# Kernel optimization log

Hardware: AMD Instinct MI355X
Metric: run time of the kernel (lower is better)

The kernel has to match this reference:

```python
import jax, jax.numpy as jnp
import numpy as np

D_MODEL = 1024
N_HEADS = 16
D_K = D_MODEL // N_HEADS
B, N_Q, N_KV = 2, 2048, 2048


def setup_inputs() -> dict:
    key = jax.random.key(0)
    ks = jax.random.split(key, 13)
    s = 1.0 / np.sqrt(D_MODEL)
    Q = jax.random.normal(ks[0], (B, N_Q, D_MODEL), dtype=jnp.float32)
    K = jax.random.normal(ks[1], (B, N_KV, D_MODEL), dtype=jnp.float32)
    V = jax.random.normal(ks[2], (B, N_KV, D_MODEL), dtype=jnp.float32)
    mask = jax.random.uniform(ks[3], (B, N_KV)) > 0.1
    mask = mask.at[:, 0].set(True)  # ensure at least one valid kv per batch
    Wq = jax.random.uniform(ks[4], (D_MODEL, D_MODEL), minval=-s, maxval=s)
    bq = jax.random.uniform(ks[5], (D_MODEL,), minval=-s, maxval=s)
    Wk = jax.random.uniform(ks[6], (D_MODEL, D_MODEL), minval=-s, maxval=s)
    bk = jax.random.uniform(ks[7], (D_MODEL,), minval=-s, maxval=s)
    Wv = jax.random.uniform(ks[8], (D_MODEL, D_MODEL), minval=-s, maxval=s)
    bv = jax.random.uniform(ks[9], (D_MODEL,), minval=-s, maxval=s)
    Wo = jax.random.uniform(ks[10], (D_MODEL, D_MODEL), minval=-s, maxval=s)
    bo = jax.random.uniform(ks[11], (D_MODEL,), minval=-s, maxval=s)
    return {"Q": Q, "K": K, "V": V, "mask": mask,
            "Wq": Wq, "bq": bq, "Wk": Wk, "bk": bk,
            "Wv": Wv, "bv": bv, "Wo": Wo, "bo": bo}


def reference(Q, K, V, mask, Wq, bq, Wk, bk, Wv, bv, Wo, bo):
    Bsz, nq, _ = Q.shape
    nkv = K.shape[1]
    # torch Linear: y = x @ W.T + b
    q = (Q @ Wq.T + bq).reshape(Bsz, nq, N_HEADS, D_K).transpose(0, 2, 1, 3)
    k = (K @ Wk.T + bk).reshape(Bsz, nkv, N_HEADS, D_K).transpose(0, 2, 1, 3)
    v = (V @ Wv.T + bv).reshape(Bsz, nkv, N_HEADS, D_K).transpose(0, 2, 1, 3)
    scores = jnp.einsum('bhqd,bhkd->bhqk', q, k) / jnp.sqrt(jnp.float32(D_K))
    scores = jnp.where(mask[:, None, None, :], scores, -jnp.inf)
    attn = jax.nn.softmax(scores, axis=-1)  # dropout p=0 (eval) -> identity
    out = jnp.einsum('bhqk,bhkd->bhqd', attn, v)
    out = out.transpose(0, 2, 1, 3).reshape(Bsz, nq, D_MODEL)
    return (out @ Wo.T + bo, attn)
```

## Files before the change

### kernel.cpp

```cpp
#include <hip/hip_runtime.h>
#include <math.h>

#define H 16
#define DK 64
#define NSEQ 2048
#define DM 1024
#define BSZ 2

typedef float f32x4 __attribute__((ext_vector_type(4)));
typedef short bf16x8 __attribute__((ext_vector_type(8)));
typedef unsigned short u16;

__device__ __forceinline__ u16 f2bf(float f) {
    unsigned int u = __float_as_uint(f);
    u += 0x7fffu + ((u >> 16) & 1u);
    return (u16)(u >> 16);
}
__device__ __forceinline__ float bf2f(u16 h) {
    return __uint_as_float(((unsigned int)h) << 16);
}

__global__ __launch_bounds__(256)
void cvt4_bf16(const float* __restrict__ s0, const float* __restrict__ s1,
               const float* __restrict__ s2, const float* __restrict__ s3,
               u16* __restrict__ dst) {
    const int sel = blockIdx.x >> 10;
    const float* s = sel == 0 ? s0 : sel == 1 ? s1 : sel == 2 ? s2 : s3;
    const int i = ((blockIdx.x & 1023) * 256 + threadIdx.x) * 4;
    float4 v = *(const float4*)(&s[i]);
    ushort4 o = make_ushort4(f2bf(v.x), f2bf(v.y), f2bf(v.z), f2bf(v.w));
    *(ushort4*)(&dst[(size_t)sel * DM * DM + i]) = o;
}

__global__ __launch_bounds__(1024, 4)
void gemm_qkv(const float* __restrict__ Qs_, const float* __restrict__ Ks_,
              const float* __restrict__ Vs_,
              const u16* __restrict__ Wqb, const u16* __restrict__ Wkb,
              const u16* __restrict__ Wvb,
              const float* __restrict__ bq, const float* __restrict__ bk,
              const float* __restrict__ bv,
              u16* __restrict__ qd, u16* __restrict__ kd, u16* __restrict__ vt) {
    __shared__ __align__(16) u16 At[64 * 1024];

    const int which = blockIdx.x >> 6;
    const int mblk  = blockIdx.x & 63;
    const float* A    = which == 0 ? Qs_ : which == 1 ? Ks_ : Vs_;
    const u16*   Wb   = which == 0 ? Wqb : which == 1 ? Wkb : Wvb;
    const float* bias = which == 0 ? bq  : which == 1 ? bk  : bv;

    const int tid  = threadIdx.x;
    const int lane = tid & 63;
    const int w    = tid >> 6;
    const int m0   = mblk * 64;

    {
        const int row = tid & 63;
        const int kg  = tid >> 6;
#pragma unroll
        for (int i = 0; i < 8; ++i) {
            int k = kg * 64 + i * 8;
            float4 a0 = *(const float4*)(&A[(size_t)(m0 + row) * 1024 + k]);
            float4 a1 = *(const float4*)(&A[(size_t)(m0 + row) * 1024 + k + 4]);
            bf16x8 pv;
            pv[0] = (short)f2bf(a0.x); pv[1] = (short)f2bf(a0.y);
            pv[2] = (short)f2bf(a0.z); pv[3] = (short)f2bf(a0.w);
            pv[4] = (short)f2bf(a1.x); pv[5] = (short)f2bf(a1.y);
            pv[6] = (short)f2bf(a1.z); pv[7] = (short)f2bf(a1.w);
            int slot = (kg * 8 + i) ^ (row & 7);
            *(bf16x8*)(&At[row * 1024 + slot * 8]) = pv;
        }
    }
    __syncthreads();

    const int fr = lane & 15;
    const int fg = lane >> 4;

    f32x4 acc[4][4];
#pragma unroll
    for (int rf = 0; rf < 4; ++rf)
#pragma unroll
        for (int ct = 0; ct < 4; ++ct) acc[rf][ct] = {0.f, 0.f, 0.f, 0.f};

    const int nbase = w * 64;
    for (int ks = 0; ks < 32; ++ks) {
        int slot = (ks * 4 + fg) ^ (fr & 7);
        bf16x8 aA[4];
#pragma unroll
        for (int rf = 0; rf < 4; ++rf)
            aA[rf] = *(const bf16x8*)(&At[(rf * 16 + fr) * 1024 + slot * 8]);
#pragma unroll
        for (int ct = 0; ct < 4; ++ct) {
            bf16x8 bB = *(const bf16x8*)(&Wb[(size_t)(nbase + ct * 16 + fr) * 1024 + ks * 32 + fg * 8]);
#pragma unroll
            for (int rf = 0; rf < 4; ++rf)
                acc[rf][ct] = __builtin_amdgcn_mfma_f32_16x16x32_bf16(aA[rf], bB, acc[rf][ct], 0, 0, 0);
        }
    }

    const int b = m0 >> 11;
    if (which == 2) {
#pragma unroll
        for (int ct = 0; ct < 4; ++ct) {
            int n = nbase + ct * 16 + fr;
            float bvv = bias[n];
            int hh = n >> 6, d = n & 63;
            size_t base = ((size_t)(b * H + hh)) * DK * NSEQ + (size_t)d * NSEQ;
#pragma unroll
            for (int rf = 0; rf < 4; ++rf) {
                int kv = (m0 & 2047) + rf * 16 + fg * 4;
                ushort4 pk = make_ushort4(f2bf(acc[rf][ct][0] + bvv), f2bf(acc[rf][ct][1] + bvv),
                                          f2bf(acc[rf][ct][2] + bvv), f2bf(acc[rf][ct][3] + bvv));
                *(ushort4*)(&vt[base + kv]) = pk;
            }
        }
    } else {
        u16* C = which == 0 ? qd : kd;
#pragma unroll
        for (int ct = 0; ct < 4; ++ct) {
            int n = nbase + ct * 16 + fr;
            float bvv = bias[n];
            int hh = n >> 6, d = n & 63;
#pragma unroll
            for (int rf = 0; rf < 4; ++rf)
#pragma unroll
                for (int reg = 0; reg < 4; ++reg) {
                    int nq = (m0 & 2047) + rf * 16 + fg * 4 + reg;
                    C[(((size_t)(b * H + hh)) * NSEQ + nq) * DK + d] = f2bf(acc[rf][ct][reg] + bvv);
                }
        }
    }
}

__global__ __launch_bounds__(256)
void gemm_out(const u16* __restrict__ Ab, const u16* __restrict__ Wb,
              const float* __restrict__ bias, float* __restrict__ Cdst) {
    __shared__ __align__(16) char smem[16 * 1028 * 4];
    u16* At = (u16*)smem;

    const int tid  = threadIdx.x;
    const int lane = tid & 63;
    const int w    = tid >> 6;
    const int m0   = blockIdx.x * 16;

    {
        const int row = tid & 15;
        const int kg  = tid >> 4;
#pragma unroll
        for (int i = 0; i < 8; ++i) {
            int k = kg * 64 + i * 8;
            bf16x8 pv = *(const bf16x8*)(&Ab[(size_t)(m0 + row) * 1024 + k]);
            int slot = (kg * 8 + i) ^ (row & 7);
            *(bf16x8*)(&At[row * 1024 + slot * 8]) = pv;
        }
    }
    __syncthreads();

    const int fr = lane & 15;
    const int fg = lane >> 4;

    f32x4 acc[16];
#pragma unroll
    for (int ct = 0; ct < 16; ++ct) acc[ct] = {0.f, 0.f, 0.f, 0.f};

    const int nbase = w * 256;
    for (int ks = 0; ks < 32; ++ks) {
        int slot = (ks * 4 + fg) ^ (fr & 7);
        bf16x8 aA = *(const bf16x8*)(&At[fr * 1024 + slot * 8]);
#pragma unroll
        for (int ct = 0; ct < 16; ++ct) {
            bf16x8 bB = *(const bf16x8*)(&Wb[(size_t)(nbase + ct * 16 + fr) * 1024 + ks * 32 + fg * 8]);
            acc[ct] = __builtin_amdgcn_mfma_f32_16x16x32_bf16(aA, bB, acc[ct], 0, 0, 0);
        }
    }

    __syncthreads();
    float* Ct = (float*)smem;
    const int r4 = fg * 4;
#pragma unroll
    for (int ct = 0; ct < 16; ++ct) {
        int n = nbase + ct * 16 + fr;
        float bvv = bias[n];
#pragma unroll
        for (int reg = 0; reg < 4; ++reg)
            Ct[(r4 + reg) * 1028 + n] = acc[ct][reg] + bvv;
    }
    __syncthreads();
#pragma unroll
    for (int rr = 0; rr < 4; ++rr) {
        int row = w * 4 + rr;
#pragma unroll
        for (int seg = 0; seg < 4; ++seg) {
            int c = seg * 256 + lane * 4;
            f32x4 v = *(const f32x4*)(&Ct[row * 1028 + c]);
            *(f32x4*)(&Cdst[(size_t)(m0 + row) * 1024 + c]) = v;
        }
    }
}

__global__ __launch_bounds__(512, 2)
void attn_mfma(const u16* __restrict__ qb, const u16* __restrict__ kb,
               const u16* __restrict__ vt, const int* __restrict__ mask,
               float* __restrict__ attn, u16* __restrict__ ao) {
    __shared__ __align__(16) u16 Pband[32][2056];
    __shared__ unsigned Mbits[64];
    __shared__ float Sws[8][32];
    __shared__ float Sinv[32];

    const int tid  = threadIdx.x;
    const int lane = tid & 63;
    const int w    = tid >> 6;
    const int fr   = lane & 15;
    const int fg   = lane >> 4;

    const int bid = blockIdx.x;
    const int wg  = (bid & 7) * 256 + (bid >> 3);
    const int bh  = wg >> 6;
    const int qt  = wg & 63;
    const int b   = bh / H, h = bh % H;
    const int q0  = qt * 32;

    const u16* qh = qb + (size_t)bh * NSEQ * DK;
    const u16* kh = kb + (size_t)bh * NSEQ * DK;
    const u16* vh = vt + (size_t)bh * DK * NSEQ;

#pragma unroll
    for (int j = 0; j < 4; ++j) {
        int kv = j * 512 + w * 64 + lane;
        unsigned long long bal = __ballot(mask[b * NSEQ + kv] != 0);
        if (lane == 0) {
            Mbits[j * 16 + w * 2]     = (unsigned)bal;
            Mbits[j * 16 + w * 2 + 1] = (unsigned)(bal >> 32);
        }
    }

    bf16x8 aQ[2][2];
#pragma unroll
    for (int qs = 0; qs < 2; ++qs)
#pragma unroll
        for (int ks = 0; ks < 2; ++ks)
            aQ[qs][ks] = *(const bf16x8*)(&qh[(size_t)(q0 + qs * 16 + fr) * DK + ks * 32 + fg * 8]);

    const int col0 = w * 32 + fr;
    const int col1 = col0 + 16;

    __syncthreads();

    unsigned mb0 = 0, mb1 = 0;
#pragma unroll
    for (int st = 0; st < 8; ++st) {
        unsigned word = Mbits[st * 8 + w];
        mb0 |= ((word >> fr) & 1u) << st;
        mb1 |= ((word >> (16 + fr)) & 1u) << st;
    }

    float sum[2][4] = {};
    f32x4 accO[2][4];
#pragma unroll
    for (int qs = 0; qs < 2; ++qs)
#pragma unroll
        for (int g = 0; g < 4; ++g) accO[qs][g] = {0.f, 0.f, 0.f, 0.f};
    const float scale = 0.125f;

    bf16x8 bK0c[2], bK1c[2];
#pragma unroll
    for (int ks = 0; ks < 2; ++ks) {
        bK0c[ks] = *(const bf16x8*)(&kh[(size_t)col0 * DK + ks * 32 + fg * 8]);
        bK1c[ks] = *(const bf16x8*)(&kh[(size_t)col1 * DK + ks * 32 + fg * 8]);
    }

    for (int st = 0; st < 8; ++st) {
        const int cb = st * 256;

        bf16x8 bV[4];
#pragma unroll
        for (int g = 0; g < 4; ++g)
            bV[g] = *(const bf16x8*)(&vh[(size_t)(g * 16 + fr) * NSEQ + cb + w * 32 + fg * 8]);

        const int stn = (st < 7) ? st + 1 : 7;
        bf16x8 bK0n[2], bK1n[2];
#pragma unroll
        for (int ks = 0; ks < 2; ++ks) {
            bK0n[ks] = *(const bf16x8*)(&kh[(size_t)(stn * 256 + col0) * DK + ks * 32 + fg * 8]);
            bK1n[ks] = *(const bf16x8*)(&kh[(size_t)(stn * 256 + col1) * DK + ks * 32 + fg * 8]);
        }

        __builtin_amdgcn_s_setprio(1);
        f32x4 s0[2], s1[2];
#pragma unroll
        for (int qs = 0; qs < 2; ++qs) { s0[qs] = {0.f,0.f,0.f,0.f}; s1[qs] = {0.f,0.f,0.f,0.f}; }
#pragma unroll
        for (int qs = 0; qs < 2; ++qs)
#pragma unroll
            for (int ks = 0; ks < 2; ++ks) {
                s0[qs] = __builtin_amdgcn_mfma_f32_16x16x32_bf16(aQ[qs][ks], bK0c[ks], s0[qs], 0, 0, 0);
                s1[qs] = __builtin_amdgcn_mfma_f32_16x16x32_bf16(aQ[qs][ks], bK1c[ks], s1[qs], 0, 0, 0);
            }
        __builtin_amdgcn_s_setprio(0);

        const bool m0 = (mb0 >> st) & 1, m1 = (mb1 >> st) & 1;
#pragma unroll
        for (int qs = 0; qs < 2; ++qs)
#pragma unroll
            for (int reg = 0; reg < 4; ++reg) {
                float e0 = m0 ? __expf(s0[qs][reg] * scale) : 0.f;
                float e1 = m1 ? __expf(s1[qs][reg] * scale) : 0.f;
                sum[qs][reg] += e0 + e1;
                Pband[qs * 16 + fg * 4 + reg][cb + col0] = f2bf(e0);
                Pband[qs * 16 + fg * 4 + reg][cb + col1] = f2bf(e1);
            }

        asm volatile("s_waitcnt lgkmcnt(0)" ::: "memory");
        bf16x8 aP[2];
#pragma unroll
        for (int qs = 0; qs < 2; ++qs)
            aP[qs] = *(const bf16x8*)(&Pband[qs * 16 + fr][cb + w * 32 + fg * 8]);

        __builtin_amdgcn_s_setprio(1);
#pragma unroll
        for (int qs = 0; qs < 2; ++qs)
#pragma unroll
            for (int g = 0; g < 4; ++g)
                accO[qs][g] = __builtin_amdgcn_mfma_f32_16x16x32_bf16(aP[qs], bV[g], accO[qs][g], 0, 0, 0);
        __builtin_amdgcn_s_setprio(0);

#pragma unroll
        for (int ks = 0; ks < 2; ++ks) { bK0c[ks] = bK0n[ks]; bK1c[ks] = bK1n[ks]; }
    }

#pragma unroll
    for (int off = 1; off < 16; off <<= 1) {
#pragma unroll
        for (int qs = 0; qs < 2; ++qs)
#pragma unroll
            for (int reg = 0; reg < 4; ++reg)
                sum[qs][reg] += __shfl_xor(sum[qs][reg], off);
    }
    if (fr == 0) {
#pragma unroll
        for (int qs = 0; qs < 2; ++qs)
#pragma unroll
            for (int reg = 0; reg < 4; ++reg)
                Sws[w][qs * 16 + fg * 4 + reg] = sum[qs][reg];
    }
    __syncthreads();
    if (tid < 32) {
        float s = 0.f;
#pragma unroll
        for (int wv = 0; wv < 8; ++wv) s += Sws[wv][tid];
        Sinv[tid] = 1.0f / s;
    }
    __syncthreads();

#pragma unroll
    for (int rr = 0; rr < 4; ++rr) {
        int row = w * 4 + rr;
        float inv = Sinv[row];
        float* dst = attn + ((size_t)bh * NSEQ + q0 + row) * NSEQ;
#pragma unroll
        for (int seg = 0; seg < 8; ++seg) {
            int c = seg * 256 + lane * 4;
            ushort4 pv = *(const ushort4*)(&Pband[row][c]);
            f32x4 o = { bf2f(pv.x) * inv, bf2f(pv.y) * inv,
                        bf2f(pv.z) * inv, bf2f(pv.w) * inv };
            *(f32x4*)(&dst[c]) = o;
        }
    }
    __syncthreads();

    float* Of = (float*)Pband;
#pragma unroll
    for (int qs = 0; qs < 2; ++qs)
#pragma unroll
        for (int g = 0; g < 4; ++g)
#pragma unroll
            for (int reg = 0; reg < 4; ++reg)
                Of[(w * 32 + qs * 16 + fg * 4 + reg) * 68 + g * 16 + fr] = accO[qs][g][reg];
    __syncthreads();
    {
        int row = tid >> 4, cq = (tid & 15) * 4;
        f32x4 o = {0.f, 0.f, 0.f, 0.f};
#pragma unroll
        for (int wv = 0; wv < 8; ++wv)
            o += *(const f32x4*)(&Of[(wv * 32 + row) * 68 + cq]);
        float inv = Sinv[row];
        ushort4 st4 = make_ushort4(f2bf(o[0] * inv), f2bf(o[1] * inv),
                                   f2bf(o[2] * inv), f2bf(o[3] * inv));
        *(ushort4*)(&ao[((size_t)(b * NSEQ + q0 + row)) * DM + h * DK + cq]) = st4;
    }
}

extern "C" void kernel_launch(void* const* d_in, const int* in_sizes, int n_in,
                              void* d_out, int out_size, void* d_ws, size_t ws_size,
                              hipStream_t stream) {
    const float* Q    = (const float*)d_in[0];
    const float* K    = (const float*)d_in[1];
    const float* V    = (const float*)d_in[2];
    const int*   mask = (const int*)  d_in[3];
    const float* Wq   = (const float*)d_in[4];
    const float* bq   = (const float*)d_in[5];
    const float* Wk   = (const float*)d_in[6];
    const float* bk   = (const float*)d_in[7];
    const float* Wv   = (const float*)d_in[8];
    const float* bv   = (const float*)d_in[9];
    const float* Wo   = (const float*)d_in[10];
    const float* bo   = (const float*)d_in[11];

    float* out  = (float*)d_out;
    float* attn = out + (size_t)BSZ * NSEQ * DM;

    u16* Wqb = (u16*)d_ws;
    u16* Wkb = Wqb + (size_t)DM * DM;
    u16* Wvb = Wkb + (size_t)DM * DM;
    u16* Wob = Wvb + (size_t)DM * DM;
    u16* qbp = Wob + (size_t)DM * DM;
    u16* kbp = qbp + (size_t)BSZ * NSEQ * DM;
    u16* vbp = kbp + (size_t)BSZ * NSEQ * DM;
    u16* aob = vbp + (size_t)BSZ * NSEQ * DM;
    u16* vtb = aob + (size_t)BSZ * NSEQ * DM;

    cvt4_bf16<<<dim3(4096), dim3(256), 0, stream>>>(Wq, Wk, Wv, Wo, Wqb);

    gemm_qkv<<<dim3(192), dim3(1024), 0, stream>>>(Q, K, V, Wqb, Wkb, Wvb,
                                                   bq, bk, bv, qbp, kbp, vtb);

    attn_mfma<<<dim3(BSZ * H * (NSEQ / 32)), dim3(512), 0, stream>>>(qbp, kbp, vtb, mask, attn, aob);

    gemm_out<<<dim3(BSZ * NSEQ / 16), dim3(256), 0, stream>>>(aob, Wob, bo, out);
}
```

Measured before the change: 375.2 us.

## Split attention into a row-sum pass and a recompute pass with a small LDS stage

Measured after the change: 415.4 us. 1.11x slower.

```diff
diff --git a/kernel.cpp b/kernel.cpp
--- a/kernel.cpp
+++ b/kernel.cpp
@@ -197,14 +197,17 @@
     }
 }
 
-__global__ __launch_bounds__(512, 2)
+#define PST 260
+__global__ __launch_bounds__(512, 4)
 void attn_mfma(const u16* __restrict__ qb, const u16* __restrict__ kb,
                const u16* __restrict__ vt, const int* __restrict__ mask,
                float* __restrict__ attn, u16* __restrict__ ao) {
-    __shared__ __align__(16) u16 Pband[32][2056];
+    __shared__ __align__(16) char lds[256 * 66 * 4];
     __shared__ unsigned Mbits[64];
     __shared__ float Sws[8][32];
     __shared__ float Sinv[32];
+
+    float* stage = (float*)lds;
 
     const int tid  = threadIdx.x;
     const int lane = tid & 63;
@@ -235,38 +238,92 @@
 
     bf16x8 aQ[2][2];
 #pragma unroll
-    for (int qs = 0; qs < 2; ++qs)
+    for (int qg = 0; qg < 2; ++qg)
 #pragma unroll
         for (int ks = 0; ks < 2; ++ks)
-            aQ[qs][ks] = *(const bf16x8*)(&qh[(size_t)(q0 + qs * 16 + fr) * DK + ks * 32 + fg * 8]);
-
-    const int col0 = w * 32 + fr;
-    const int col1 = col0 + 16;
-
-    __syncthreads();
-
-    unsigned mb0 = 0, mb1 = 0;
-#pragma unroll
-    for (int st = 0; st < 8; ++st) {
-        unsigned word = Mbits[st * 8 + w];
-        mb0 |= ((word >> fr) & 1u) << st;
-        mb1 |= ((word >> (16 + fr)) & 1u) << st;
-    }
-
-    float sum[2][4] = {};
+            aQ[qg][ks] = *(const bf16x8*)(&qh[(size_t)(q0 + qg * 16 + fr) * DK + ks * 32 + fg * 8]);
+
+    __syncthreads();
+
+    const float scale = 0.125f;
+    const int slab = w * 32;
+
+    float sum[2] = {0.f, 0.f};
+    {
+        bf16x8 aKc[2][2], aKn[2][2];
+#pragma unroll
+        for (int kvb = 0; kvb < 2; ++kvb)
+#pragma unroll
+            for (int ks = 0; ks < 2; ++ks)
+                aKc[kvb][ks] = *(const bf16x8*)(&kh[(size_t)(slab + kvb * 16 + fr) * DK + ks * 32 + fg * 8]);
+
+        for (int st = 0; st < 8; ++st) {
+            const int stn = (st < 7) ? st + 1 : 7;
+#pragma unroll
+            for (int kvb = 0; kvb < 2; ++kvb)
+#pragma unroll
+                for (int ks = 0; ks < 2; ++ks)
+                    aKn[kvb][ks] = *(const bf16x8*)(&kh[(size_t)(stn * 256 + slab + kvb * 16 + fr) * DK + ks * 32 + fg * 8]);
+
+            __builtin_amdgcn_s_setprio(1);
+            f32x4 s[2][2];
+#pragma unroll
+            for (int qg = 0; qg < 2; ++qg)
+#pragma unroll
+                for (int kvb = 0; kvb < 2; ++kvb) {
+                    s[qg][kvb] = {0.f, 0.f, 0.f, 0.f};
+#pragma unroll
+                    for (int ks = 0; ks < 2; ++ks)
+                        s[qg][kvb] = __builtin_amdgcn_mfma_f32_16x16x32_bf16(aKc[kvb][ks], aQ[qg][ks], s[qg][kvb], 0, 0, 0);
+                }
+            __builtin_amdgcn_s_setprio(0);
+
+            const unsigned word = Mbits[st * 8 + w];
+#pragma unroll
+            for (int qg = 0; qg < 2; ++qg)
+#pragma unroll
+                for (int kvb = 0; kvb < 2; ++kvb)
+#pragma unroll
+                    for (int reg = 0; reg < 4; ++reg) {
+                        bool mm = (word >> (kvb * 16 + fg * 4 + reg)) & 1u;
+                        sum[qg] += mm ? __expf(s[qg][kvb][reg] * scale) : 0.f;
+                    }
+#pragma unroll
+            for (int kvb = 0; kvb < 2; ++kvb)
+#pragma unroll
+                for (int ks = 0; ks < 2; ++ks) aKc[kvb][ks] = aKn[kvb][ks];
+        }
+    }
+
+#pragma unroll
+    for (int off = 16; off < 64; off <<= 1) {
+#pragma unroll
+        for (int qg = 0; qg < 2; ++qg)
+            sum[qg] += __shfl_xor(sum[qg], off);
+    }
+    if (fg == 0) {
+#pragma unroll
+        for (int qg = 0; qg < 2; ++qg)
+            Sws[w][qg * 16 + fr] = sum[qg];
+    }
+    __syncthreads();
+    if (tid < 32) {
+        float s = 0.f;
+#pragma unroll
+        for (int wv = 0; wv < 8; ++wv) s += Sws[wv][tid];
+        Sinv[tid] = 1.0f / s;
+    }
+    __syncthreads();
+
+    float sinv[2];
+#pragma unroll
+    for (int qg = 0; qg < 2; ++qg) sinv[qg] = Sinv[qg * 16 + fr];
+
     f32x4 accO[2][4];
 #pragma unroll
-    for (int qs = 0; qs < 2; ++qs)
-#pragma unroll
-        for (int g = 0; g < 4; ++g) accO[qs][g] = {0.f, 0.f, 0.f, 0.f};
-    const float scale = 0.125f;
-
-    bf16x8 bK0c[2], bK1c[2];
-#pragma unroll
-    for (int ks = 0; ks < 2; ++ks) {
-        bK0c[ks] = *(const bf16x8*)(&kh[(size_t)col0 * DK + ks * 32 + fg * 8]);
-        bK1c[ks] = *(const bf16x8*)(&kh[(size_t)col1 * DK + ks * 32 + fg * 8]);
-    }
+    for (int qg = 0; qg < 2; ++qg)
+#pragma unroll
+        for (int g = 0; g < 4; ++g) accO[qg][g] = {0.f, 0.f, 0.f, 0.f};
 
     for (int st = 0; st < 8; ++st) {
         const int cb = st * 256;
@@ -274,117 +331,91 @@
         bf16x8 bV[4];
 #pragma unroll
         for (int g = 0; g < 4; ++g)
-            bV[g] = *(const bf16x8*)(&vh[(size_t)(g * 16 + fr) * NSEQ + cb + w * 32 + fg * 8]);
-
-        const int stn = (st < 7) ? st + 1 : 7;
-        bf16x8 bK0n[2], bK1n[2];
-#pragma unroll
-        for (int ks = 0; ks < 2; ++ks) {
-            bK0n[ks] = *(const bf16x8*)(&kh[(size_t)(stn * 256 + col0) * DK + ks * 32 + fg * 8]);
-            bK1n[ks] = *(const bf16x8*)(&kh[(size_t)(stn * 256 + col1) * DK + ks * 32 + fg * 8]);
-        }
+            bV[g] = *(const bf16x8*)(&vh[(size_t)(g * 16 + fr) * NSEQ + cb + slab + fg * 8]);
+
+        bf16x8 aK[2][2];
+#pragma unroll
+        for (int kvb = 0; kvb < 2; ++kvb)
+#pragma unroll
+            for (int ks = 0; ks < 2; ++ks)
+                aK[kvb][ks] = *(const bf16x8*)(&kh[(size_t)(cb + slab + kvb * 16 + fr) * DK + ks * 32 + fg * 8]);
 
         __builtin_amdgcn_s_setprio(1);
-        f32x4 s0[2], s1[2];
-#pragma unroll
-        for (int qs = 0; qs < 2; ++qs) { s0[qs] = {0.f,0.f,0.f,0.f}; s1[qs] = {0.f,0.f,0.f,0.f}; }
-#pragma unroll
-        for (int qs = 0; qs < 2; ++qs)
-#pragma unroll
-            for (int ks = 0; ks < 2; ++ks) {
-                s0[qs] = __builtin_amdgcn_mfma_f32_16x16x32_bf16(aQ[qs][ks], bK0c[ks], s0[qs], 0, 0, 0);
-                s1[qs] = __builtin_amdgcn_mfma_f32_16x16x32_bf16(aQ[qs][ks], bK1c[ks], s1[qs], 0, 0, 0);
+        f32x4 s[2][2];
+#pragma unroll
+        for (int qg = 0; qg < 2; ++qg)
+#pragma unroll
+            for (int kvb = 0; kvb < 2; ++kvb) {
+                s[qg][kvb] = {0.f, 0.f, 0.f, 0.f};
+#pragma unroll
+                for (int ks = 0; ks < 2; ++ks)
+                    s[qg][kvb] = __builtin_amdgcn_mfma_f32_16x16x32_bf16(aK[kvb][ks], aQ[qg][ks], s[qg][kvb], 0, 0, 0);
             }
         __builtin_amdgcn_s_setprio(0);
 
-        const bool m0 = (mb0 >> st) & 1, m1 = (mb1 >> st) & 1;
-#pragma unroll
-        for (int qs = 0; qs < 2; ++qs)
-#pragma unroll
-            for (int reg = 0; reg < 4; ++reg) {
-                float e0 = m0 ? __expf(s0[qs][reg] * scale) : 0.f;
-                float e1 = m1 ? __expf(s1[qs][reg] * scale) : 0.f;
-                sum[qs][reg] += e0 + e1;
-                Pband[qs * 16 + fg * 4 + reg][cb + col0] = f2bf(e0);
-                Pband[qs * 16 + fg * 4 + reg][cb + col1] = f2bf(e1);
+        const unsigned word = Mbits[st * 8 + w];
+#pragma unroll
+        for (int qg = 0; qg < 2; ++qg) {
+            const int row = qg * 16 + fr;
+            const int sw  = (row & 7) << 2;
+#pragma unroll
+            for (int kvb = 0; kvb < 2; ++kvb) {
+                f32x4 ev;
+#pragma unroll
+                for (int reg = 0; reg < 4; ++reg) {
+                    bool mm = (word >> (kvb * 16 + fg * 4 + reg)) & 1u;
+                    ev[reg] = mm ? __expf(s[qg][kvb][reg] * scale) * sinv[qg] : 0.f;
+                }
+                int col = (slab + kvb * 16 + fg * 4) ^ sw;
+                *(f32x4*)(&stage[row * PST + col]) = ev;
             }
-
-        asm volatile("s_waitcnt lgkmcnt(0)" ::: "memory");
-        bf16x8 aP[2];
-#pragma unroll
-        for (int qs = 0; qs < 2; ++qs)
-            aP[qs] = *(const bf16x8*)(&Pband[qs * 16 + fr][cb + w * 32 + fg * 8]);
+        }
+        __syncthreads();
+
+#pragma unroll
+        for (int rr = 0; rr < 4; ++rr) {
+            int row = w * 4 + rr;
+            int sw  = (row & 7) << 2;
+            f32x4 v = *(const f32x4*)(&stage[row * PST + ((lane * 4) ^ sw)]);
+            *(f32x4*)(&attn[((size_t)bh * NSEQ + q0 + row) * NSEQ + cb + lane * 4]) = v;
+        }
 
         __builtin_amdgcn_s_setprio(1);
 #pragma unroll
-        for (int qs = 0; qs < 2; ++qs)
+        for (int qg = 0; qg < 2; ++qg) {
+            const int row = qg * 16 + fr;
+            const int sw  = (row & 7) << 2;
+            f32x4 p0 = *(const f32x4*)(&stage[row * PST + ((slab + fg * 8) ^ sw)]);
+            f32x4 p1 = *(const f32x4*)(&stage[row * PST + ((slab + fg * 8 + 4) ^ sw)]);
+            bf16x8 aP;
+            aP[0] = (short)f2bf(p0[0]); aP[1] = (short)f2bf(p0[1]);
+            aP[2] = (short)f2bf(p0[2]); aP[3] = (short)f2bf(p0[3]);
+            aP[4] = (short)f2bf(p1[0]); aP[5] = (short)f2bf(p1[1]);
+            aP[6] = (short)f2bf(p1[2]); aP[7] = (short)f2bf(p1[3]);
 #pragma unroll
             for (int g = 0; g < 4; ++g)
-                accO[qs][g] = __builtin_amdgcn_mfma_f32_16x16x32_bf16(aP[qs], bV[g], accO[qs][g], 0, 0, 0);
+                accO[qg][g] = __builtin_amdgcn_mfma_f32_16x16x32_bf16(aP, bV[g], accO[qg][g], 0, 0, 0);
+        }
         __builtin_amdgcn_s_setprio(0);
-
-#pragma unroll
-        for (int ks = 0; ks < 2; ++ks) { bK0c[ks] = bK0n[ks]; bK1c[ks] = bK1n[ks]; }
-    }
-
-#pragma unroll
-    for (int off = 1; off < 16; off <<= 1) {
-#pragma unroll
-        for (int qs = 0; qs < 2; ++qs)
+        __syncthreads();
+    }
+
+    float* Of = (float*)lds;
+#pragma unroll
+    for (int qg = 0; qg < 2; ++qg)
+#pragma unroll
+        for (int g = 0; g < 4; ++g)
 #pragma unroll
             for (int reg = 0; reg < 4; ++reg)
-                sum[qs][reg] += __shfl_xor(sum[qs][reg], off);
-    }
-    if (fr == 0) {
-#pragma unroll
-        for (int qs = 0; qs < 2; ++qs)
-#pragma unroll
-            for (int reg = 0; reg < 4; ++reg)
-                Sws[w][qs * 16 + fg * 4 + reg] = sum[qs][reg];
-    }
-    __syncthreads();
-    if (tid < 32) {
-        float s = 0.f;
-#pragma unroll
-        for (int wv = 0; wv < 8; ++wv) s += Sws[wv][tid];
-        Sinv[tid] = 1.0f / s;
-    }
-    __syncthreads();
-
-#pragma unroll
-    for (int rr = 0; rr < 4; ++rr) {
-        int row = w * 4 + rr;
-        float inv = Sinv[row];
-        float* dst = attn + ((size_t)bh * NSEQ + q0 + row) * NSEQ;
-#pragma unroll
-        for (int seg = 0; seg < 8; ++seg) {
-            int c = seg * 256 + lane * 4;
-            ushort4 pv = *(const ushort4*)(&Pband[row][c]);
-            f32x4 o = { bf2f(pv.x) * inv, bf2f(pv.y) * inv,
-                        bf2f(pv.z) * inv, bf2f(pv.w) * inv };
-            *(f32x4*)(&dst[c]) = o;
-        }
-    }
-    __syncthreads();
-
-    float* Of = (float*)Pband;
-#pragma unroll
-    for (int qs = 0; qs < 2; ++qs)
-#pragma unroll
-        for (int g = 0; g < 4; ++g)
-#pragma unroll
-            for (int reg = 0; reg < 4; ++reg)
-                Of[(w * 32 + qs * 16 + fg * 4 + reg) * 68 + g * 16 + fr] = accO[qs][g][reg];
+                Of[(w * 32 + qg * 16 + fg * 4 + reg) * 66 + g * 16 + fr] = accO[qg][g][reg];
     __syncthreads();
     {
         int row = tid >> 4, cq = (tid & 15) * 4;
         f32x4 o = {0.f, 0.f, 0.f, 0.f};
 #pragma unroll
         for (int wv = 0; wv < 8; ++wv)
-            o += *(const f32x4*)(&Of[(wv * 32 + row) * 68 + cq]);
-        float inv = Sinv[row];
-        ushort4 st4 = make_ushort4(f2bf(o[0] * inv), f2bf(o[1] * inv),
-                                   f2bf(o[2] * inv), f2bf(o[3] * inv));
+            o += *(const f32x4*)(&Of[(wv * 32 + row) * 66 + cq]);
+        ushort4 st4 = make_ushort4(f2bf(o[0]), f2bf(o[1]), f2bf(o[2]), f2bf(o[3]));
         *(ushort4*)(&ao[((size_t)(b * NSEQ + q0 + row)) * DM + h * DK + cq]) = st4;
     }
 }
```
